# Kernel optimization log

Hardware: AMD Instinct MI355X
Metric: run time of the kernel (lower is better)

Reference implementation:

```python
import jax, jax.numpy as jnp
import numpy as np

B, S, D_MODEL, H = 2, 2048, 768, 12
HD = D_MODEL // H  # head_dim = 64
EPS = 1e-5


def setup_inputs() -> dict:
    key = jax.random.key(0)
    ks = jax.random.split(key, 5)
    sc = 0.02
    return {
        "x": jax.random.normal(ks[0], (B, S, D_MODEL), dtype=jnp.float32),
        "Wproj_w": jax.random.normal(ks[1], (7 * D_MODEL, D_MODEL), dtype=jnp.float32) * sc,
        "Wproj_b": jax.random.normal(ks[2], (7 * D_MODEL,), dtype=jnp.float32) * sc,
        "gn_w": jnp.ones((D_MODEL,), dtype=jnp.float32),
        "gn_b": jnp.zeros((D_MODEL,), dtype=jnp.float32),
        "out_w": jax.random.normal(ks[3], (D_MODEL, D_MODEL), dtype=jnp.float32) * sc,
        "out_b": jax.random.normal(ks[4], (D_MODEL,), dtype=jnp.float32) * sc,
    }


def _time_swiglu(qkv):
    # qkv: [B, S, 7, H, D]
    q1, k1, q2, k2, q3, k3, v = [qkv[:, :, i] for i in range(7)]
    a1 = jnp.einsum('bthd,bshd->bhts', q1, k1)  # [B,H,S,S], raw scores, no softmax
    a2 = jnp.einsum('bthd,bshd->bhts', q2, k2)
    a3 = jnp.einsum('bthd,bshd->bhts', q3, k3)
    t1 = jax.nn.silu(jnp.einsum('bhts,bshd->bthd', a1, v))
    t2 = jnp.einsum('bhts,bshd->bthd', a2, v)
    return jnp.einsum('bhts,bshd->bthd', a3, t1 * t2)  # [B,S,H,D]


def _group_norm(ctx, gn_w, gn_b):
    # ctx: [B, S, D_MODEL]; torch applies GroupNorm(H, D_MODEL) over (B, C=D_MODEL, L=S)
    g = ctx.reshape(B, S, H, HD)
    mean = jnp.mean(g, axis=(1, 3), keepdims=True)          # per (batch, group) over (S, HD)
    var = jnp.var(g, axis=(1, 3), keepdims=True)
    g = (g - mean) * jax.lax.rsqrt(var + EPS)
    g = g.reshape(B, S, D_MODEL)
    return g * gn_w + gn_b


def reference(x, Wproj_w, Wproj_b, gn_w, gn_b, out_w, out_b):
    qkv = x @ Wproj_w.T + Wproj_b                  # [B,S,7*D_MODEL]
    qkv = qkv.reshape(B, S, 7, H, HD)
    ctx = _time_swiglu(qkv).reshape(B, S, D_MODEL)  # [B,S,D_MODEL]
    ctx = _group_norm(ctx, gn_w, gn_b)
    return ctx @ out_w.T + out_b
```

## Files before the change

kernel.cpp:

```cpp
#include <hip/hip_runtime.h>
#include <hip/hip_bf16.h>
#include <stdint.h>

typedef short short8 __attribute__((ext_vector_type(8)));
typedef float f32x4 __attribute__((ext_vector_type(4)));
typedef float f32x16 __attribute__((ext_vector_type(16)));
typedef unsigned short u16x4 __attribute__((ext_vector_type(4)));
typedef unsigned uint4v __attribute__((ext_vector_type(4)));

#define MFMA16 __builtin_amdgcn_mfma_f32_16x16x32_bf16
#define MFMA32 __builtin_amdgcn_mfma_f32_32x32x16_bf16

typedef unsigned int __attribute__((address_space(1))) as1_u32;
typedef unsigned int __attribute__((address_space(3))) as3_u32;
#define GLOAD16(gsrc, ldst) \
  __builtin_amdgcn_global_load_lds((const as1_u32*)(gsrc), (as3_u32*)(ldst), 16, 0, 0)

__device__ __forceinline__ unsigned short f2bf(float f) {
  __hip_bfloat16 h = __float2bfloat16(f);
  return *(unsigned short*)&h;
}
__device__ __forceinline__ unsigned pk2(float lo, float hi) {
  return ((unsigned)f2bf(hi) << 16) | (unsigned)f2bf(lo);
}
__device__ __forceinline__ void plswap(unsigned &a, unsigned &b) {
  asm volatile("v_permlane32_swap_b32 %0, %1" : "+v"(a), "+v"(b));
}

__device__ __forceinline__ short8 pv_frag(const f32x16* acc, int kc2) {
  int n = kc2 >> 1, c = kc2 & 1;
  int o0 = 2 * c, o1 = 2 * c + 1;
  unsigned x0 = pk2(acc[n][o0 * 4 + 0], acc[n][o0 * 4 + 1]);
  unsigned x1 = pk2(acc[n][o0 * 4 + 2], acc[n][o0 * 4 + 3]);
  unsigned y0 = pk2(acc[n][o1 * 4 + 0], acc[n][o1 * 4 + 1]);
  unsigned y1 = pk2(acc[n][o1 * 4 + 2], acc[n][o1 * 4 + 3]);
  plswap(x0, y0);
  plswap(x1, y1);
  uint4v fu; fu.x = x0; fu.y = x1; fu.z = y0; fu.w = y1;
  return __builtin_bit_cast(short8, fu);
}

__global__ __launch_bounds__(256) void cvt_bf16_4(const float* __restrict__ in,
                                                  unsigned short* __restrict__ out,
                                                  int n) {
  int i = (blockIdx.x * 256 + threadIdx.x) * 4;
  if (i >= n) return;
  f32x4 v = *(const f32x4*)(in + i);
  u16x4 o;
  o.x = f2bf(v.x); o.y = f2bf(v.y); o.z = f2bf(v.z); o.w = f2bf(v.w);
  *(u16x4*)(out + i) = o;
}

__global__ __launch_bounds__(256) void transp64(const unsigned short* __restrict__ src,
                                                int stride, int off,
                                                unsigned short* __restrict__ dst) {
  __shared__ __align__(16) unsigned short t[64 * 64];
  const int tid = threadIdx.x;
  const int tt = blockIdx.x, bh = blockIdx.y;
  const int b = bh / 12, h = bh % 12;
  const unsigned short* sbase = src + (size_t)(b * 2048 + tt * 64) * stride + h * 64 + off;
  for (int it = 0; it < 2; ++it) {
    int slot = it * 256 + tid, s = slot >> 3, j = slot & 7;
    short8 v = *(const short8*)(sbase + (size_t)s * stride + j * 8);
    int phys = (s + 8 * j) & 63;
    for (int e = 0; e < 8; ++e)
      t[(j * 8 + e) * 64 + phys] = ((unsigned short*)&v)[e];
  }
  __syncthreads();
  unsigned short* dbase = dst + (size_t)bh * 64 * 2048 + tt * 64;
  for (int it = 0; it < 2; ++it) {
    int slot = it * 256 + tid, d = slot >> 3, c = slot & 7;
    int pc = (c + (d >> 3)) & 7;
    short8 v = *(const short8*)(t + d * 64 + pc * 8);
    *(short8*)(dbase + (size_t)d * 2048 + c * 8) = v;
  }
}

template <bool OUT_BF16>
__global__ __launch_bounds__(256) void gemm_nt(const unsigned short* __restrict__ A,
                                               const unsigned short* __restrict__ Bm,
                                               const float* __restrict__ bias,
                                               void* __restrict__ Cout,
                                               int M, int N, int K) {
  __shared__ __align__(16) char smem[32768];
  char* As = smem;
  char* Bs = smem + 16384;
  const int tid = threadIdx.x;
  const int w = tid >> 6, l = tid & 63;
  const int wm = w >> 1, wn = w & 1;
  const int Row0 = blockIdx.y * 128, Col0 = blockIdx.x * 128;

  f32x4 z; z.x = 0.f; z.y = 0.f; z.z = 0.f; z.w = 0.f;
  f32x4 acc[4][4];
  for (int m = 0; m < 4; ++m)
    for (int n = 0; n < 4; ++n) acc[m][n] = z;

  for (int k0 = 0; k0 < K; k0 += 64) {
    for (int it = 0; it < 4; ++it) {
      int slot = it * 256 + tid;
      int row = slot >> 3, j = slot & 7;
      int gc = j ^ (row & 7);
      GLOAD16(A + (size_t)(Row0 + row) * K + k0 + gc * 8, As + slot * 16);
      GLOAD16(Bm + (size_t)(Col0 + row) * K + k0 + gc * 8, Bs + slot * 16);
    }
    __syncthreads();
    for (int kc = 0; kc < 2; ++kc) {
      int c = (l >> 4) + 4 * kc;
      short8 af[4], bf[4];
      for (int m = 0; m < 4; ++m) {
        int t = wm * 64 + m * 16 + (l & 15);
        af[m] = *(const short8*)(As + t * 128 + ((c ^ (t & 7)) * 16));
      }
      for (int n = 0; n < 4; ++n) {
        int t = wn * 64 + n * 16 + (l & 15);
        bf[n] = *(const short8*)(Bs + t * 128 + ((c ^ (t & 7)) * 16));
      }
      for (int m = 0; m < 4; ++m)
        for (int n = 0; n < 4; ++n)
          acc[m][n] = MFMA16(af[m], bf[n], acc[m][n], 0, 0, 0);
    }
    __syncthreads();
  }
  for (int n = 0; n < 4; ++n) {
    int col = Col0 + wn * 64 + n * 16 + (l & 15);
    float bv = bias[col];
    for (int m = 0; m < 4; ++m) {
      int rbase = Row0 + wm * 64 + m * 16 + (l >> 4) * 4;
      for (int r = 0; r < 4; ++r) {
        float v = acc[m][n][r] + bv;
        size_t idx = (size_t)(rbase + r) * N + col;
        if (OUT_BF16) ((unsigned short*)Cout)[idx] = f2bf(v);
        else          ((float*)Cout)[idx] = v;
      }
    }
  }
}

__global__ __launch_bounds__(128) void pass1(const unsigned short* __restrict__ qkv,
                                             const unsigned short* __restrict__ vt,
                                             unsigned short* __restrict__ u) {
  __shared__ __align__(16) char smem[49152];
  const int tid = threadIdx.x, w = tid >> 6, l = tid & 63;
  const int g5 = l >> 5, l31 = l & 31;
  const int tt = blockIdx.x, bh = blockIdx.y;
  const int b = bh / 12, h = bh % 12;
  const int matOff = (w == 0) ? 0 : 2 * 768;

  short8 qf[2][4];
#pragma unroll
  for (int tc = 0; tc < 2; ++tc) {
    const unsigned short* qrow =
        qkv + (size_t)(b * 2048 + tt * 64 + tc * 32 + l31) * 5376 + h * 64 + matOff;
#pragma unroll
    for (int kc = 0; kc < 4; ++kc)
      qf[tc][kc] = *(const short8*)(qrow + kc * 16 + g5 * 8);
  }

  f32x16 z16;
#pragma unroll
  for (int i = 0; i < 16; ++i) z16[i] = 0.f;
  f32x16 tacc[2][2];
  tacc[0][0] = z16; tacc[0][1] = z16; tacc[1][0] = z16; tacc[1][1] = z16;

  auto STAGE = [&](char* buf, int s0) {
#pragma unroll
    for (int c = 0; c < 4; ++c) {
      int r = c * 128 + tid, row = r >> 3, j = r & 7, gc = j ^ (row & 7);
      GLOAD16(qkv + (size_t)(b * 2048 + s0 + row) * 5376 + h * 64 + 1 * 768 + gc * 8,
              buf + r * 16);
    }
#pragma unroll
    for (int c = 0; c < 4; ++c) {
      int r = c * 128 + tid, row = r >> 3, j = r & 7, gc = j ^ (row & 7);
      GLOAD16(qkv + (size_t)(b * 2048 + s0 + row) * 5376 + h * 64 + 3 * 768 + gc * 8,
              buf + 8192 + r * 16);
    }
#pragma unroll
    for (int c = 0; c < 4; ++c) {
      int r = c * 128 + tid, row = r >> 3, j = r & 7, gc = j ^ (row & 7);
      GLOAD16(vt + (size_t)(bh * 64 + row) * 2048 + s0 + gc * 8, buf + 16384 + r * 16);
    }
  };

  STAGE(smem, 0);
  __syncthreads();
  for (int si = 0; si < 32; ++si) {
    char* cur = smem + (si & 1) * 24576;
    if (si < 31) STAGE(smem + ((si + 1) & 1) * 24576, (si + 1) * 64);
    const char* Ks = cur + w * 8192;
    const char* Vs = cur + 16384;

    f32x16 at[2][2];
    at[0][0] = z16; at[0][1] = z16; at[1][0] = z16; at[1][1] = z16;
#pragma unroll
    for (int kc = 0; kc < 4; ++kc)
#pragma unroll
      for (int sn = 0; sn < 2; ++sn) {
        int srow = sn * 32 + l31;
        short8 kf = *(const short8*)(Ks + srow * 128 + (((kc * 2 + g5) ^ (l31 & 7)) * 16));
        at[0][sn] = MFMA32(kf, qf[0][kc], at[0][sn], 0, 0, 0);
        at[1][sn] = MFMA32(kf, qf[1][kc], at[1][sn], 0, 0, 0);
      }
#pragma unroll
    for (int kc2 = 0; kc2 < 4; ++kc2) {
      short8 pa0 = pv_frag(at[0], kc2);
      short8 pa1 = pv_frag(at[1], kc2);
#pragma unroll
      for (int dn = 0; dn < 2; ++dn) {
        int drow = dn * 32 + l31;
        short8 vf = *(const short8*)(Vs + drow * 128 + (((kc2 * 2 + g5) ^ (l31 & 7)) * 16));
        tacc[0][dn] = MFMA32(pa0, vf, tacc[0][dn], 0, 0, 0);
        tacc[1][dn] = MFMA32(pa1, vf, tacc[1][dn], 0, 0, 0);
      }
    }
    __syncthreads();
  }

  float* exch = (float*)smem;
  if (w == 1) {
#pragma unroll
    for (int tc = 0; tc < 2; ++tc)
#pragma unroll
      for (int dn = 0; dn < 2; ++dn)
#pragma unroll
        for (int r = 0; r < 16; ++r) {
          int trow = tc * 32 + (r & 3) + 8 * (r >> 2) + 4 * g5;
          exch[trow * 64 + dn * 32 + l31] = tacc[tc][dn][r];
        }
  }
  __syncthreads();
  if (w == 0) {
#pragma unroll
    for (int tc = 0; tc < 2; ++tc)
#pragma unroll
      for (int dn = 0; dn < 2; ++dn)
#pragma unroll
        for (int r = 0; r < 16; ++r) {
          int crow = (r & 3) + 8 * (r >> 2) + 4 * g5;
          int t = tt * 64 + tc * 32 + crow;
          int d = dn * 32 + l31;
          float x1 = tacc[tc][dn][r];
          float x2 = exch[(tc * 32 + crow) * 64 + d];
          float uu = (x1 / (1.f + expf(-x1))) * x2;
          u[(size_t)(b * 2048 + t) * 768 + h * 64 + d] = f2bf(uu);
        }
  }
}

__global__ __launch_bounds__(128) void pass2(const unsigned short* __restrict__ qkv,
                                             const unsigned short* __restrict__ ut,
                                             float* __restrict__ ctx,
                                             float* __restrict__ partials) {
  __shared__ __align__(16) char smem[32768];
  const int tid = threadIdx.x, w = tid >> 6, l = tid & 63;
  const int g5 = l >> 5, l31 = l & 31;
  const int tt = blockIdx.x, bh = blockIdx.y;
  const int b = bh / 12, h = bh % 12;

  short8 qf[2][4];
#pragma unroll
  for (int tc = 0; tc < 2; ++tc) {
    const unsigned short* qrow =
        qkv + (size_t)(b * 2048 + tt * 64 + tc * 32 + l31) * 5376 + h * 64 + 4 * 768;
#pragma unroll
    for (int kc = 0; kc < 4; ++kc)
      qf[tc][kc] = *(const short8*)(qrow + kc * 16 + g5 * 8);
  }

  f32x16 z16;
#pragma unroll
  for (int i = 0; i < 16; ++i) z16[i] = 0.f;
  f32x16 ca[2];
  ca[0] = z16; ca[1] = z16;

  auto STAGE = [&](char* buf, int s0) {
#pragma unroll
    for (int c = 0; c < 4; ++c) {
      int r = c * 128 + tid, row = r >> 3, j = r & 7, gc = j ^ (row & 7);
      GLOAD16(qkv + (size_t)(b * 2048 + s0 + row) * 5376 + h * 64 + 5 * 768 + gc * 8,
              buf + r * 16);
    }
#pragma unroll
    for (int c = 0; c < 4; ++c) {
      int r = c * 128 + tid, row = r >> 3, j = r & 7, gc = j ^ (row & 7);
      GLOAD16(ut + (size_t)(bh * 64 + row) * 2048 + s0 + gc * 8, buf + 8192 + r * 16);
    }
  };

  STAGE(smem, 0);
  __syncthreads();
  for (int si = 0; si < 32; ++si) {
    char* cur = smem + (si & 1) * 16384;
    if (si < 31) STAGE(smem + ((si + 1) & 1) * 16384, (si + 1) * 64);
    const char* Ks = cur;
    const char* Us = cur + 8192;

    f32x16 at[2][2];
    at[0][0] = z16; at[0][1] = z16; at[1][0] = z16; at[1][1] = z16;
#pragma unroll
    for (int kc = 0; kc < 4; ++kc)
#pragma unroll
      for (int sn = 0; sn < 2; ++sn) {
        int srow = sn * 32 + l31;
        short8 kf = *(const short8*)(Ks + srow * 128 + (((kc * 2 + g5) ^ (l31 & 7)) * 16));
        at[0][sn] = MFMA32(kf, qf[0][kc], at[0][sn], 0, 0, 0);
        at[1][sn] = MFMA32(kf, qf[1][kc], at[1][sn], 0, 0, 0);
      }
#pragma unroll
    for (int kc2 = 0; kc2 < 4; ++kc2) {
      short8 pa0 = pv_frag(at[0], kc2);
      short8 pa1 = pv_frag(at[1], kc2);
      int drow = w * 32 + l31;
      short8 uf = *(const short8*)(Us + drow * 128 + (((kc2 * 2 + g5) ^ (l31 & 7)) * 16));
      ca[0] = MFMA32(pa0, uf, ca[0], 0, 0, 0);
      ca[1] = MFMA32(pa1, uf, ca[1], 0, 0, 0);
    }
    __syncthreads();
  }

  float psum = 0.f, psum2 = 0.f;
#pragma unroll
  for (int tc = 0; tc < 2; ++tc)
#pragma unroll
    for (int r = 0; r < 16; ++r) {
      int t = tt * 64 + tc * 32 + (r & 3) + 8 * (r >> 2) + 4 * g5;
      int d = w * 32 + l31;
      float v = ca[tc][r];
      ctx[(size_t)(b * 2048 + t) * 768 + h * 64 + d] = v;
      psum += v; psum2 += v * v;
    }

  float* red = (float*)smem;
  red[tid] = psum; red[128 + tid] = psum2;
  __syncthreads();
  for (int st = 64; st > 0; st >>= 1) {
    if (tid < st) {
      red[tid] += red[tid + st];
      red[128 + tid] += red[128 + tid + st];
    }
    __syncthreads();
  }
  if (tid == 0) {
    partials[(bh * 32 + tt) * 2] = red[0];
    partials[(bh * 32 + tt) * 2 + 1] = red[128];
  }
}

__global__ __launch_bounds__(64) void gn_finalize(const float* __restrict__ partials,
                                                  float* __restrict__ stats) {
  const int g = blockIdx.x;
  const int l = threadIdx.x;
  double s = 0.0, s2 = 0.0;
  if (l < 32) {
    s = (double)partials[(g * 32 + l) * 2];
    s2 = (double)partials[(g * 32 + l) * 2 + 1];
  }
  for (int off = 32; off > 0; off >>= 1) {
    s += __shfl_down(s, off, 64);
    s2 += __shfl_down(s2, off, 64);
  }
  if (l == 0) {
    const double N = 2048.0 * 64.0;
    double mean = s / N;
    double var = s2 / N - mean * mean;
    stats[g * 2] = (float)mean;
    stats[g * 2 + 1] = (float)(1.0 / sqrt(var + 1e-5));
  }
}

__global__ __launch_bounds__(256) void gn_apply(const float* __restrict__ ctx,
                                                const float* __restrict__ stats,
                                                const float* __restrict__ gw,
                                                const float* __restrict__ gb,
                                                unsigned short* __restrict__ outc) {
  int i = blockIdx.x * 256 + threadIdx.x;
  if (i >= 4096 * 768) return;
  int c = i % 768;
  int b = i / (2048 * 768);
  int g = b * 12 + (c >> 6);
  float v = (ctx[i] - stats[2 * g]) * stats[2 * g + 1];
  outc[i] = f2bf(v * gw[c] + gb[c]);
}

extern "C" void kernel_launch(void* const* d_in, const int* in_sizes, int n_in,
                              void* d_out, int out_size, void* d_ws, size_t ws_size,
                              hipStream_t stream) {
  const float* x   = (const float*)d_in[0];
  const float* Wpw = (const float*)d_in[1];
  const float* Wpb = (const float*)d_in[2];
  const float* gnw = (const float*)d_in[3];
  const float* gnb = (const float*)d_in[4];
  const float* ow  = (const float*)d_in[5];
  const float* ob  = (const float*)d_in[6];
  float* out = (float*)d_out;

  char* ws = (char*)d_ws;
  size_t off = 0;
  auto carve = [&](size_t bytes) {
    char* p = ws + off;
    off = (off + bytes + 255) & ~(size_t)255;
    return p;
  };
  unsigned short* xb   = (unsigned short*)carve((size_t)4096 * 768 * 2);
  unsigned short* wb   = (unsigned short*)carve((size_t)5376 * 768 * 2);
  unsigned short* owb  = (unsigned short*)carve((size_t)768 * 768 * 2);
  unsigned short* qkvb = (unsigned short*)carve((size_t)4096 * 5376 * 2);
  unsigned short* ub   = (unsigned short*)carve((size_t)4096 * 768 * 2);
  unsigned short* vtb  = (unsigned short*)carve((size_t)24 * 64 * 2048 * 2);
  unsigned short* utb  = (unsigned short*)carve((size_t)24 * 64 * 2048 * 2);
  float* ctx           = (float*)carve((size_t)4096 * 768 * 4);
  float* partials      = (float*)carve(24 * 32 * 2 * 4);
  float* stats         = (float*)carve(48 * 4);

  cvt_bf16_4<<<3072, 256, 0, stream>>>(x, xb, 4096 * 768);
  cvt_bf16_4<<<4032, 256, 0, stream>>>(Wpw, wb, 5376 * 768);
  cvt_bf16_4<<<576, 256, 0, stream>>>(ow, owb, 768 * 768);

  gemm_nt<true><<<dim3(42, 32), 256, 0, stream>>>(xb, wb, Wpb, qkvb, 4096, 5376, 768);
  transp64<<<dim3(32, 24), 256, 0, stream>>>(qkvb, 5376, 6 * 768, vtb);
  pass1<<<dim3(32, 24), 128, 0, stream>>>(qkvb, vtb, ub);
  transp64<<<dim3(32, 24), 256, 0, stream>>>(ub, 768, 0, utb);
  pass2<<<dim3(32, 24), 128, 0, stream>>>(qkvb, utb, ctx, partials);
  gn_finalize<<<24, 64, 0, stream>>>(partials, stats);
  gn_apply<<<12288, 256, 0, stream>>>(ctx, stats, gnw, gnb, xb);
  gemm_nt<false><<<dim3(6, 32), 256, 0, stream>>>(xb, owb, ob, out, 4096, 768, 768);
}
```

Measured before the change: 241.2 us.

## Split key sequence across more waves in attention passes with cross-wave reduction

pass1 and pass2 now launch 256 threads per block instead of 128. Each wave handles a different slice of the key/sequence dimension: two halves in pass1 and four quarters in pass2, with smaller 32-row tiles per step. The partial accumulators are summed through shared memory at the end. This raises the number of waves per block to improve latency hiding and MFMA occupancy on the same grid. In exchange it adds LDS reduction traffic and extra barriers, and pass2 drops double-buffered staging in favour of a synchronous load per step.

```diff
diff --git a/kernel.cpp b/kernel.cpp
--- a/kernel.cpp
+++ b/kernel.cpp
@@ -136,24 +136,24 @@
   }
 }
 
-__global__ __launch_bounds__(128) void pass1(const unsigned short* __restrict__ qkv,
+__global__ __launch_bounds__(256) void pass1(const unsigned short* __restrict__ qkv,
                                              const unsigned short* __restrict__ vt,
                                              unsigned short* __restrict__ u) {
   __shared__ __align__(16) char smem[49152];
   const int tid = threadIdx.x, w = tid >> 6, l = tid & 63;
+  const int m = w & 1, sh = w >> 1;
   const int g5 = l >> 5, l31 = l & 31;
   const int tt = blockIdx.x, bh = blockIdx.y;
   const int b = bh / 12, h = bh % 12;
-  const int matOff = (w == 0) ? 0 : 2 * 768;
 
   short8 qf[2][4];
 #pragma unroll
-  for (int tc = 0; tc < 2; ++tc) {
+  for (int tb = 0; tb < 2; ++tb) {
     const unsigned short* qrow =
-        qkv + (size_t)(b * 2048 + tt * 64 + tc * 32 + l31) * 5376 + h * 64 + matOff;
+        qkv + (size_t)(b * 2048 + tt * 64 + tb * 32 + l31) * 5376 + h * 64 + m * 2 * 768;
 #pragma unroll
     for (int kc = 0; kc < 4; ++kc)
-      qf[tc][kc] = *(const short8*)(qrow + kc * 16 + g5 * 8);
+      qf[tb][kc] = *(const short8*)(qrow + kc * 16 + g5 * 8);
   }
 
   f32x16 z16;
@@ -162,92 +162,125 @@
   f32x16 tacc[2][2];
   tacc[0][0] = z16; tacc[0][1] = z16; tacc[1][0] = z16; tacc[1][1] = z16;
 
-  auto STAGE = [&](char* buf, int s0) {
-#pragma unroll
-    for (int c = 0; c < 4; ++c) {
-      int r = c * 128 + tid, row = r >> 3, j = r & 7, gc = j ^ (row & 7);
-      GLOAD16(qkv + (size_t)(b * 2048 + s0 + row) * 5376 + h * 64 + 1 * 768 + gc * 8,
-              buf + r * 16);
-    }
-#pragma unroll
-    for (int c = 0; c < 4; ++c) {
-      int r = c * 128 + tid, row = r >> 3, j = r & 7, gc = j ^ (row & 7);
-      GLOAD16(qkv + (size_t)(b * 2048 + s0 + row) * 5376 + h * 64 + 3 * 768 + gc * 8,
-              buf + 8192 + r * 16);
-    }
-#pragma unroll
-    for (int c = 0; c < 4; ++c) {
-      int r = c * 128 + tid, row = r >> 3, j = r & 7, gc = j ^ (row & 7);
-      GLOAD16(vt + (size_t)(bh * 64 + row) * 2048 + s0 + gc * 8, buf + 16384 + r * 16);
+  auto STAGE = [&](char* buf, int si) {
+#pragma unroll
+    for (int shs = 0; shs < 2; ++shs) {
+      int s0 = shs * 1024 + si * 32;
+      char* hb = buf + shs * 12288;
+      {
+        int row = tid >> 3, pc = tid & 7, gc = pc ^ (row & 7);
+        const unsigned short* base =
+            qkv + (size_t)(b * 2048 + s0 + row) * 5376 + h * 64 + gc * 8;
+        GLOAD16(base + 768, hb + tid * 16);
+        GLOAD16(base + 3 * 768, hb + 4096 + tid * 16);
+      }
+      {
+        int row = tid >> 2, pc = tid & 3, gc = pc ^ ((row >> 1) & 3);
+        GLOAD16(vt + (size_t)(bh * 64 + row) * 2048 + s0 + gc * 8,
+                hb + 8192 + tid * 16);
+      }
     }
   };
 
   STAGE(smem, 0);
   __syncthreads();
   for (int si = 0; si < 32; ++si) {
-    char* cur = smem + (si & 1) * 24576;
-    if (si < 31) STAGE(smem + ((si + 1) & 1) * 24576, (si + 1) * 64);
-    const char* Ks = cur + w * 8192;
-    const char* Vs = cur + 16384;
-
-    f32x16 at[2][2];
-    at[0][0] = z16; at[0][1] = z16; at[1][0] = z16; at[1][1] = z16;
+    const char* cur = smem + (si & 1) * 24576 + sh * 12288;
+    if (si < 31) STAGE(smem + ((si + 1) & 1) * 24576, si + 1);
+    const char* Ks = cur + m * 4096;
+    const char* Vs = cur + 8192;
+
+    short8 kreg[4], vreg[4];
 #pragma unroll
     for (int kc = 0; kc < 4; ++kc)
-#pragma unroll
-      for (int sn = 0; sn < 2; ++sn) {
-        int srow = sn * 32 + l31;
-        short8 kf = *(const short8*)(Ks + srow * 128 + (((kc * 2 + g5) ^ (l31 & 7)) * 16));
-        at[0][sn] = MFMA32(kf, qf[0][kc], at[0][sn], 0, 0, 0);
-        at[1][sn] = MFMA32(kf, qf[1][kc], at[1][sn], 0, 0, 0);
-      }
-#pragma unroll
-    for (int kc2 = 0; kc2 < 4; ++kc2) {
-      short8 pa0 = pv_frag(at[0], kc2);
-      short8 pa1 = pv_frag(at[1], kc2);
+      kreg[kc] = *(const short8*)(Ks + l31 * 128 + (((kc * 2 + g5) ^ (l31 & 7)) * 16));
+#pragma unroll
+    for (int kc2 = 0; kc2 < 2; ++kc2)
 #pragma unroll
       for (int dn = 0; dn < 2; ++dn) {
-        int drow = dn * 32 + l31;
-        short8 vf = *(const short8*)(Vs + drow * 128 + (((kc2 * 2 + g5) ^ (l31 & 7)) * 16));
-        tacc[0][dn] = MFMA32(pa0, vf, tacc[0][dn], 0, 0, 0);
-        tacc[1][dn] = MFMA32(pa1, vf, tacc[1][dn], 0, 0, 0);
+        int drow = dn * 32 + l31, c = kc2 * 2 + g5;
+        vreg[kc2 * 2 + dn] =
+            *(const short8*)(Vs + drow * 64 + ((c ^ ((drow >> 1) & 3)) * 16));
+      }
+
+#pragma unroll
+    for (int tb = 0; tb < 2; ++tb) {
+      f32x16 a = z16;
+#pragma unroll
+      for (int kc = 0; kc < 4; ++kc)
+        a = MFMA32(kreg[kc], qf[tb][kc], a, 0, 0, 0);
+#pragma unroll
+      for (int kc2 = 0; kc2 < 2; ++kc2) {
+        short8 pa = pv_frag(&a, kc2);
+#pragma unroll
+        for (int dn = 0; dn < 2; ++dn)
+          tacc[tb][dn] = MFMA32(pa, vreg[kc2 * 2 + dn], tacc[tb][dn], 0, 0, 0);
       }
     }
     __syncthreads();
   }
 
-  float* exch = (float*)smem;
-  if (w == 1) {
-#pragma unroll
-    for (int tc = 0; tc < 2; ++tc)
+  float* ex = (float*)smem;
+  if (sh == 1) {
+#pragma unroll
+    for (int tb = 0; tb < 2; ++tb)
+#pragma unroll
+      for (int dn = 0; dn < 2; ++dn)
+#pragma unroll
+        for (int qd = 0; qd < 4; ++qd) {
+          f32x4 v;
+          v.x = tacc[tb][dn][qd * 4 + 0]; v.y = tacc[tb][dn][qd * 4 + 1];
+          v.z = tacc[tb][dn][qd * 4 + 2]; v.w = tacc[tb][dn][qd * 4 + 3];
+          *(f32x4*)((char*)ex + m * 16384 + ((tb * 2 + dn) * 4 + qd) * 1024 + l * 16) = v;
+        }
+  }
+  __syncthreads();
+  if (sh == 0) {
+#pragma unroll
+    for (int tb = 0; tb < 2; ++tb)
+#pragma unroll
+      for (int dn = 0; dn < 2; ++dn)
+#pragma unroll
+        for (int qd = 0; qd < 4; ++qd) {
+          f32x4 v = *(const f32x4*)((char*)ex + m * 16384 +
+                                    ((tb * 2 + dn) * 4 + qd) * 1024 + l * 16);
+          tacc[tb][dn][qd * 4 + 0] += v.x; tacc[tb][dn][qd * 4 + 1] += v.y;
+          tacc[tb][dn][qd * 4 + 2] += v.z; tacc[tb][dn][qd * 4 + 3] += v.w;
+        }
+  }
+  __syncthreads();
+  if (sh == 0 && m == 1) {
+#pragma unroll
+    for (int tb = 0; tb < 2; ++tb)
+#pragma unroll
+      for (int dn = 0; dn < 2; ++dn)
+#pragma unroll
+        for (int qd = 0; qd < 4; ++qd) {
+          f32x4 v;
+          v.x = tacc[tb][dn][qd * 4 + 0]; v.y = tacc[tb][dn][qd * 4 + 1];
+          v.z = tacc[tb][dn][qd * 4 + 2]; v.w = tacc[tb][dn][qd * 4 + 3];
+          *(f32x4*)((char*)ex + ((tb * 2 + dn) * 4 + qd) * 1024 + l * 16) = v;
+        }
+  }
+  __syncthreads();
+  if (sh == 0 && m == 0) {
+#pragma unroll
+    for (int tb = 0; tb < 2; ++tb)
 #pragma unroll
       for (int dn = 0; dn < 2; ++dn)
 #pragma unroll
         for (int r = 0; r < 16; ++r) {
-          int trow = tc * 32 + (r & 3) + 8 * (r >> 2) + 4 * g5;
-          exch[trow * 64 + dn * 32 + l31] = tacc[tc][dn][r];
-        }
-  }
-  __syncthreads();
-  if (w == 0) {
-#pragma unroll
-    for (int tc = 0; tc < 2; ++tc)
-#pragma unroll
-      for (int dn = 0; dn < 2; ++dn)
-#pragma unroll
-        for (int r = 0; r < 16; ++r) {
-          int crow = (r & 3) + 8 * (r >> 2) + 4 * g5;
-          int t = tt * 64 + tc * 32 + crow;
+          float x2 = ex[((tb * 2 + dn) * 4 + (r >> 2)) * 256 + l * 4 + (r & 3)];
+          int t = tt * 64 + tb * 32 + (r & 3) + 8 * (r >> 2) + 4 * g5;
           int d = dn * 32 + l31;
-          float x1 = tacc[tc][dn][r];
-          float x2 = exch[(tc * 32 + crow) * 64 + d];
+          float x1 = tacc[tb][dn][r];
           float uu = (x1 / (1.f + expf(-x1))) * x2;
           u[(size_t)(b * 2048 + t) * 768 + h * 64 + d] = f2bf(uu);
         }
   }
 }
 
-__global__ __launch_bounds__(128) void pass2(const unsigned short* __restrict__ qkv,
+__global__ __launch_bounds__(256) void pass2(const unsigned short* __restrict__ qkv,
                                              const unsigned short* __restrict__ ut,
                                              float* __restrict__ ctx,
                                              float* __restrict__ partials) {
@@ -259,90 +292,132 @@
 
   short8 qf[2][4];
 #pragma unroll
-  for (int tc = 0; tc < 2; ++tc) {
+  for (int tb = 0; tb < 2; ++tb) {
     const unsigned short* qrow =
-        qkv + (size_t)(b * 2048 + tt * 64 + tc * 32 + l31) * 5376 + h * 64 + 4 * 768;
+        qkv + (size_t)(b * 2048 + tt * 64 + tb * 32 + l31) * 5376 + h * 64 + 4 * 768;
 #pragma unroll
     for (int kc = 0; kc < 4; ++kc)
-      qf[tc][kc] = *(const short8*)(qrow + kc * 16 + g5 * 8);
+      qf[tb][kc] = *(const short8*)(qrow + kc * 16 + g5 * 8);
   }
 
   f32x16 z16;
 #pragma unroll
   for (int i = 0; i < 16; ++i) z16[i] = 0.f;
-  f32x16 ca[2];
-  ca[0] = z16; ca[1] = z16;
-
-  auto STAGE = [&](char* buf, int s0) {
-#pragma unroll
-    for (int c = 0; c < 4; ++c) {
-      int r = c * 128 + tid, row = r >> 3, j = r & 7, gc = j ^ (row & 7);
-      GLOAD16(qkv + (size_t)(b * 2048 + s0 + row) * 5376 + h * 64 + 5 * 768 + gc * 8,
-              buf + r * 16);
-    }
-#pragma unroll
-    for (int c = 0; c < 4; ++c) {
-      int r = c * 128 + tid, row = r >> 3, j = r & 7, gc = j ^ (row & 7);
-      GLOAD16(ut + (size_t)(bh * 64 + row) * 2048 + s0 + gc * 8, buf + 8192 + r * 16);
+  f32x16 ca[2][2];
+  ca[0][0] = z16; ca[0][1] = z16; ca[1][0] = z16; ca[1][1] = z16;
+
+  auto STAGE = [&](int si) {
+#pragma unroll
+    for (int qs = 0; qs < 4; ++qs) {
+      int s0 = qs * 512 + si * 32;
+      char* hb = smem + qs * 8192;
+      {
+        int row = tid >> 3, pc = tid & 7, gc = pc ^ (row & 7);
+        GLOAD16(qkv + (size_t)(b * 2048 + s0 + row) * 5376 + h * 64 + 5 * 768 + gc * 8,
+                hb + tid * 16);
+      }
+      {
+        int row = tid >> 2, pc = tid & 3, gc = pc ^ ((row >> 1) & 3);
+        GLOAD16(ut + (size_t)(bh * 64 + row) * 2048 + s0 + gc * 8,
+                hb + 4096 + tid * 16);
+      }
     }
   };
 
-  STAGE(smem, 0);
-  __syncthreads();
-  for (int si = 0; si < 32; ++si) {
-    char* cur = smem + (si & 1) * 16384;
-    if (si < 31) STAGE(smem + ((si + 1) & 1) * 16384, (si + 1) * 64);
-    const char* Ks = cur;
-    const char* Us = cur + 8192;
-
-    f32x16 at[2][2];
-    at[0][0] = z16; at[0][1] = z16; at[1][0] = z16; at[1][1] = z16;
+  for (int si = 0; si < 16; ++si) {
+    STAGE(si);
+    __syncthreads();
+    const char* Ks = smem + w * 8192;
+    const char* Us = Ks + 4096;
+
+    short8 kreg[4], ureg[4];
 #pragma unroll
     for (int kc = 0; kc < 4; ++kc)
-#pragma unroll
-      for (int sn = 0; sn < 2; ++sn) {
-        int srow = sn * 32 + l31;
-        short8 kf = *(const short8*)(Ks + srow * 128 + (((kc * 2 + g5) ^ (l31 & 7)) * 16));
-        at[0][sn] = MFMA32(kf, qf[0][kc], at[0][sn], 0, 0, 0);
-        at[1][sn] = MFMA32(kf, qf[1][kc], at[1][sn], 0, 0, 0);
-      }
-#pragma unroll
-    for (int kc2 = 0; kc2 < 4; ++kc2) {
-      short8 pa0 = pv_frag(at[0], kc2);
-      short8 pa1 = pv_frag(at[1], kc2);
-      int drow = w * 32 + l31;
-      short8 uf = *(const short8*)(Us + drow * 128 + (((kc2 * 2 + g5) ^ (l31 & 7)) * 16));
-      ca[0] = MFMA32(pa0, uf, ca[0], 0, 0, 0);
-      ca[1] = MFMA32(pa1, uf, ca[1], 0, 0, 0);
+      kreg[kc] = *(const short8*)(Ks + l31 * 128 + (((kc * 2 + g5) ^ (l31 & 7)) * 16));
+#pragma unroll
+    for (int kc2 = 0; kc2 < 2; ++kc2)
+#pragma unroll
+      for (int dn = 0; dn < 2; ++dn) {
+        int drow = dn * 32 + l31, c = kc2 * 2 + g5;
+        ureg[kc2 * 2 + dn] =
+            *(const short8*)(Us + drow * 64 + ((c ^ ((drow >> 1) & 3)) * 16));
+      }
+
+#pragma unroll
+    for (int tb = 0; tb < 2; ++tb) {
+      f32x16 a = z16;
+#pragma unroll
+      for (int kc = 0; kc < 4; ++kc)
+        a = MFMA32(kreg[kc], qf[tb][kc], a, 0, 0, 0);
+#pragma unroll
+      for (int kc2 = 0; kc2 < 2; ++kc2) {
+        short8 pa = pv_frag(&a, kc2);
+#pragma unroll
+        for (int dn = 0; dn < 2; ++dn)
+          ca[tb][dn] = MFMA32(pa, ureg[kc2 * 2 + dn], ca[tb][dn], 0, 0, 0);
+      }
     }
     __syncthreads();
   }
 
+  float* ex = (float*)smem;
+  auto DUMP = [&](int region) {
+#pragma unroll
+    for (int tb = 0; tb < 2; ++tb)
+#pragma unroll
+      for (int dn = 0; dn < 2; ++dn)
+#pragma unroll
+        for (int qd = 0; qd < 4; ++qd) {
+          f32x4 v;
+          v.x = ca[tb][dn][qd * 4 + 0]; v.y = ca[tb][dn][qd * 4 + 1];
+          v.z = ca[tb][dn][qd * 4 + 2]; v.w = ca[tb][dn][qd * 4 + 3];
+          *(f32x4*)((char*)ex + region * 16384 + ((tb * 2 + dn) * 4 + qd) * 1024 + l * 16) = v;
+        }
+  };
+  auto ACCUM = [&](int region) {
+#pragma unroll
+    for (int tb = 0; tb < 2; ++tb)
+#pragma unroll
+      for (int dn = 0; dn < 2; ++dn)
+#pragma unroll
+        for (int qd = 0; qd < 4; ++qd) {
+          f32x4 v = *(const f32x4*)((char*)ex + region * 16384 +
+                                    ((tb * 2 + dn) * 4 + qd) * 1024 + l * 16);
+          ca[tb][dn][qd * 4 + 0] += v.x; ca[tb][dn][qd * 4 + 1] += v.y;
+          ca[tb][dn][qd * 4 + 2] += v.z; ca[tb][dn][qd * 4 + 3] += v.w;
+        }
+  };
+  if (w == 1) DUMP(0);
+  if (w == 3) DUMP(1);
+  __syncthreads();
+  if (w == 0) ACCUM(0);
+  if (w == 2) ACCUM(1);
+  __syncthreads();
+  if (w == 2) DUMP(0);
+  __syncthreads();
   float psum = 0.f, psum2 = 0.f;
-#pragma unroll
-  for (int tc = 0; tc < 2; ++tc)
-#pragma unroll
-    for (int r = 0; r < 16; ++r) {
-      int t = tt * 64 + tc * 32 + (r & 3) + 8 * (r >> 2) + 4 * g5;
-      int d = w * 32 + l31;
-      float v = ca[tc][r];
-      ctx[(size_t)(b * 2048 + t) * 768 + h * 64 + d] = v;
-      psum += v; psum2 += v * v;
-    }
-
-  float* red = (float*)smem;
-  red[tid] = psum; red[128 + tid] = psum2;
-  __syncthreads();
-  for (int st = 64; st > 0; st >>= 1) {
-    if (tid < st) {
-      red[tid] += red[tid + st];
-      red[128 + tid] += red[128 + tid + st];
-    }
-    __syncthreads();
-  }
-  if (tid == 0) {
-    partials[(bh * 32 + tt) * 2] = red[0];
-    partials[(bh * 32 + tt) * 2 + 1] = red[128];
+  if (w == 0) {
+    ACCUM(0);
+#pragma unroll
+    for (int tb = 0; tb < 2; ++tb)
+#pragma unroll
+      for (int dn = 0; dn < 2; ++dn)
+#pragma unroll
+        for (int r = 0; r < 16; ++r) {
+          int t = tt * 64 + tb * 32 + (r & 3) + 8 * (r >> 2) + 4 * g5;
+          int d = dn * 32 + l31;
+          float v = ca[tb][dn][r];
+          ctx[(size_t)(b * 2048 + t) * 768 + h * 64 + d] = v;
+          psum += v; psum2 += v * v;
+        }
+    for (int off = 32; off > 0; off >>= 1) {
+      psum += __shfl_down(psum, off, 64);
+      psum2 += __shfl_down(psum2, off, 64);
+    }
+    if (l == 0) {
+      partials[(bh * 32 + tt) * 2] = psum;
+      partials[(bh * 32 + tt) * 2 + 1] = psum2;
+    }
   }
 }
 
@@ -418,9 +493,9 @@
 
   gemm_nt<true><<<dim3(42, 32), 256, 0, stream>>>(xb, wb, Wpb, qkvb, 4096, 5376, 768);
   transp64<<<dim3(32, 24), 256, 0, stream>>>(qkvb, 5376, 6 * 768, vtb);
-  pass1<<<dim3(32, 24), 128, 0, stream>>>(qkvb, vtb, ub);
+  pass1<<<dim3(32, 24), 256, 0, stream>>>(qkvb, vtb, ub);
   transp64<<<dim3(32, 24), 256, 0, stream>>>(ub, 768, 0, utb);
-  pass2<<<dim3(32, 24), 128, 0, stream>>>(qkvb, utb, ctx, partials);
+  pass2<<<dim3(32, 24), 256, 0, stream>>>(qkvb, utb, ctx, partials);
   gn_finalize<<<24, 64, 0, stream>>>(partials, stats);
   gn_apply<<<12288, 256, 0, stream>>>(ctx, stats, gnw, gnb, xb);
   gemm_nt<false><<<dim3(6, 32), 256, 0, stream>>>(xb, owb, ob, out, 4096, 768, 768);
```

Result: faster. 227.4 us (-5.7%).
